# Kernel optimization log

Measured on AMD Instinct MI355X. Metric: run time of the kernel, lower is better.

Reference implementation:

```python
import jax, jax.numpy as jnp
import numpy as np

HIDDEN = 4096
N_HEADS = 16
HEAD_DIM = HIDDEN // N_HEADS  # 256
ROTARY_DIM = 64
ROPE_THETA = 10000.0


def _rope_cos_sin(positions):
    # positions: [S] int -> cos/sin: [S, ROTARY_DIM//2]
    inv_freq = 1.0 / (ROPE_THETA ** (jnp.arange(0, ROTARY_DIM, 2, dtype=jnp.float32) / ROTARY_DIM))
    angles = positions.astype(jnp.float32)[:, None] * inv_freq[None, :]
    return jnp.cos(angles), jnp.sin(angles)


def _apply_rope_interleaved(x, cos, sin):
    # x: [B, S, H, D]; rotate first ROTARY_DIM dims, GPT-J (non-neox) interleaved pairs
    xr = x[..., :ROTARY_DIM]
    x1 = xr[..., 0::2]
    x2 = xr[..., 1::2]
    c = cos[None, :, None, :]
    s = sin[None, :, None, :]
    o1 = x1 * c - x2 * s
    o2 = x1 * s + x2 * c
    rot = jnp.stack([o1, o2], axis=-1).reshape(xr.shape)
    return jnp.concatenate([rot, x[..., ROTARY_DIM:]], axis=-1)


def setup_inputs() -> dict:
    key = jax.random.key(0)
    k1, k2, k3 = jax.random.split(key, 3)
    B, S = 2, 2048
    hidden_states = jax.random.normal(k1, (B, S, HIDDEN), dtype=jnp.float32)
    positions = jnp.arange(S, dtype=jnp.int32)
    w_qkv = jax.random.normal(k2, (3 * HIDDEN, HIDDEN), dtype=jnp.float32) * 0.02
    w_out = jax.random.normal(k3, (HIDDEN, HIDDEN), dtype=jnp.float32) * 0.02
    return {"hidden_states": hidden_states, "positions": positions, "w_qkv": w_qkv, "w_out": w_out}


def reference(hidden_states, positions, w_qkv, w_out):
    B, S, H = hidden_states.shape
    qkv = jnp.einsum("bsh,oh->bso", hidden_states, w_qkv)  # [B,S,3H]
    q, k, v = jnp.split(qkv, 3, axis=-1)
    q = q.reshape(B, S, N_HEADS, HEAD_DIM)
    k = k.reshape(B, S, N_HEADS, HEAD_DIM)
    v = v.reshape(B, S, N_HEADS, HEAD_DIM)
    cos, sin = _rope_cos_sin(positions)
    q = _apply_rope_interleaved(q, cos, sin)
    k = _apply_rope_interleaved(k, cos, sin)
    scale = HEAD_DIM ** -0.5
    scores = jnp.einsum("bqhd,bkhd->bhqk", q, k) * scale  # [B,nh,S,S]
    causal = jnp.tril(jnp.ones((S, S), dtype=bool))
    scores = jnp.where(causal[None, None], scores, jnp.finfo(scores.dtype).min)
    probs = jax.nn.softmax(scores, axis=-1)
    attn = jnp.einsum("bhqk,bkhd->bqhd", probs, v).reshape(B, S, H)
    return jnp.einsum("bsh,oh->bso", attn, w_out)
```

## Files before the change

kernel.cpp:

```cpp
#include <hip/hip_runtime.h>

typedef __attribute__((ext_vector_type(8))) short short8;
typedef __attribute__((ext_vector_type(4))) float f32x4;

__device__ __forceinline__ unsigned short f2bf(float f) {
    union { float f; unsigned int u; } v; v.f = f;
    unsigned int u = v.u;
    unsigned int r = (u + 0x7FFFu + ((u >> 16) & 1u)) >> 16;
    return (unsigned short)r;
}
__device__ __forceinline__ float bf2f(unsigned short u) {
    union { unsigned int u; float f; } v; v.u = ((unsigned int)u) << 16;
    return v.f;
}
__device__ __forceinline__ void load_lds16(const void* g, void* l) {
    __builtin_amdgcn_global_load_lds(
        (const __attribute__((address_space(1))) void*)g,
        (__attribute__((address_space(3))) void*)l, 16, 0, 0);
}
#define BAR() asm volatile("s_barrier" ::: "memory")
#define WAITV(n) asm volatile("s_waitcnt vmcnt(" #n ")" ::: "memory")

__device__ __forceinline__ int swz(int o) { return o ^ ((o >> 3) & 0x70); }

__global__ __launch_bounds__(256) void conv_bf16(const float* __restrict__ in,
                                                 unsigned short* __restrict__ out, int n4) {
    int i = blockIdx.x * 256 + threadIdx.x;
    if (i >= n4) return;
    float4 v = ((const float4*)in)[i];
    ushort4 o;
    o.x = f2bf(v.x); o.y = f2bf(v.y); o.z = f2bf(v.z); o.w = f2bf(v.w);
    ((ushort4*)out)[i] = o;
}

template <bool OUT_BF16>
__global__ __launch_bounds__(512, 2) void gemm256(const unsigned short* __restrict__ A,
                                                  const unsigned short* __restrict__ B,
                                                  void* __restrict__ Cv,
                                                  int M, int N, int K, int NBN) {
    __shared__ __align__(16) char smem[131072];
    const int tid = threadIdx.x;
    const int lane = tid & 63, wv = tid >> 6;
    const int wm = wv >> 2, wn = wv & 3;
    const int fr = lane & 15, fo = (lane >> 4) * 8;

    const int nwg = gridDim.x, bid = blockIdx.x;
    const int q = nwg >> 3, r = nwg & 7, xcd = bid & 7, lid = bid >> 3;
    const int wg = (xcd < r ? xcd * (q + 1) : r * (q + 1) + (xcd - r) * q) + lid;
    const int bm = wg / NBN, bn = wg % NBN;

    const unsigned short* gA = A + (size_t)bm * 256 * K;
    const unsigned short* gB = B + (size_t)bn * 256 * K;

    int srow[2][2], scol[2][2];
#pragma unroll
    for (int h = 0; h < 2; ++h)
#pragma unroll
        for (int rr = 0; rr < 2; ++rr) {
            int o = h * 16384 + rr * 8192 + tid * 16;
            int osw = swz(o);
            srow[h][rr] = osw >> 7;
            scol[h][rr] = (osw & 127) >> 1;
        }

    f32x4 acc[8][4] = {};
    short8 a[4][2], b[4][2];

    auto STAGE = [&](const unsigned short* g, int regionBase, int h, int t) {
#pragma unroll
        for (int rr = 0; rr < 2; ++rr)
            load_lds16(g + (size_t)srow[h][rr] * K + t * 64 + scol[h][rr],
                       smem + regionBase + h * 16384 + rr * 8192 + tid * 16);
    };
    auto RDA = [&](int bufBase, int mh) {
#pragma unroll
        for (int mf = 0; mf < 4; ++mf)
#pragma unroll
            for (int ks = 0; ks < 2; ++ks) {
                int o = swz((wm * 128 + mh * 64 + mf * 16 + fr) * 128 + (ks * 32 + fo) * 2);
                a[mf][ks] = *(const short8*)(smem + bufBase + o);
            }
    };
    auto RDB = [&](int bufBase, int nh) {
#pragma unroll
        for (int jj = 0; jj < 2; ++jj)
#pragma unroll
            for (int ks = 0; ks < 2; ++ks) {
                int o = swz((wn * 64 + (nh * 2 + jj) * 16 + fr) * 128 + (ks * 32 + fo) * 2);
                b[nh * 2 + jj][ks] = *(const short8*)(smem + bufBase + 32768 + o);
            }
    };
    auto MM = [&](int mh, int nh) {
        __builtin_amdgcn_s_setprio(1);
#pragma unroll
        for (int mf = 0; mf < 4; ++mf)
#pragma unroll
            for (int jj = 0; jj < 2; ++jj)
#pragma unroll
                for (int ks = 0; ks < 2; ++ks)
                    acc[mh * 4 + mf][nh * 2 + jj] = __builtin_amdgcn_mfma_f32_16x16x32_bf16(
                        a[mf][ks], b[nh * 2 + jj][ks], acc[mh * 4 + mf][nh * 2 + jj], 0, 0, 0);
        __builtin_amdgcn_s_setprio(0);
    };

    const int A0 = 0, B0 = 32768, A1 = 65536, B1 = 98304;

    STAGE(gA, A0, 0, 0); STAGE(gA, A0, 1, 0);
    STAGE(gB, B0, 0, 0); STAGE(gB, B0, 1, 0);
    STAGE(gB, B1, 0, 1); STAGE(gB, B1, 1, 1);
    STAGE(gA, A1, 0, 1); STAGE(gA, A1, 1, 1);
    WAITV(8);
    BAR();
    RDA(A0, 0);
    RDB(A0, 0);

    const int NIT = K >> 7;
    for (int i = 0; i < NIT; ++i) {
        const bool last = (i == NIT - 1);
        const int t2 = 2 * i + 2, t3 = 2 * i + 3;
        RDB(A0, 1);
        MM(0, 0);
        if (i > 0) STAGE(gA, A1, 1, 2 * i + 1);
        BAR();
        MM(0, 1);
        RDA(A0, 1);
        BAR();
        MM(1, 1);
        if (!last) {
            STAGE(gB, B0, 0, t2);
            WAITV(2);
        } else {
            WAITV(0);
        }
        BAR();
        MM(1, 0);
        RDA(A1, 0); RDB(A1, 0);
        if (!last) { STAGE(gB, B0, 1, t2); STAGE(gA, A0, 0, t2); }
        BAR();
        RDB(A1, 1);
        MM(0, 0);
        if (!last) STAGE(gA, A0, 1, t2);
        BAR();
        MM(0, 1);
        RDA(A1, 1);
        BAR();
        MM(1, 1);
        if (!last) {
            STAGE(gB, B1, 0, t3);
            WAITV(2);
        }
        BAR();
        MM(1, 0);
        if (!last) {
            RDA(A0, 0); RDB(A0, 0);
            STAGE(gB, B1, 1, t3); STAGE(gA, A1, 0, t3);
        }
        BAR();
    }

    const size_t row0 = (size_t)bm * 256 + wm * 128 + ((lane >> 4) << 2);
    const int col0 = bn * 256 + wn * 64 + fr;
#pragma unroll
    for (int mf = 0; mf < 8; ++mf)
#pragma unroll
        for (int nf = 0; nf < 4; ++nf)
#pragma unroll
            for (int j = 0; j < 4; ++j) {
                size_t idx = (row0 + mf * 16 + j) * (size_t)N + col0 + nf * 16;
                if (OUT_BF16) ((unsigned short*)Cv)[idx] = f2bf(acc[mf][nf][j]);
                else          ((float*)Cv)[idx] = acc[mf][nf][j];
            }
}

__global__ __launch_bounds__(256) void rope_repack(const unsigned short* __restrict__ qkv,
                                                   const int* __restrict__ positions,
                                                   unsigned short* __restrict__ qp,
                                                   unsigned short* __restrict__ kp) {
    int r = blockIdx.x * 4 + (threadIdx.x >> 6);
    int h = r & 15, s = (r >> 4) & 2047, b = r >> 15;
    int d = (threadIdx.x & 63) * 4;
    const unsigned short* src = qkv + (size_t)(b * 2048 + s) * 12288 + h * 256 + d;
    ushort4 q = *(const ushort4*)src;
    ushort4 k = *(const ushort4*)(src + 4096);
    if (d < 64) {
        float pos = (float)positions[s];
        const float LF = 0.4152410118609203f;
        float i0 = (float)(d >> 1);
        float a0 = pos * exp2f(-i0 * LF);
        float a1 = pos * exp2f(-(i0 + 1.0f) * LF);
        float c0 = cosf(a0), s0 = sinf(a0), c1 = cosf(a1), s1 = sinf(a1);
        float qx = bf2f(q.x), qy = bf2f(q.y), qz = bf2f(q.z), qw = bf2f(q.w);
        q.x = f2bf(qx * c0 - qy * s0); q.y = f2bf(qx * s0 + qy * c0);
        q.z = f2bf(qz * c1 - qw * s1); q.w = f2bf(qz * s1 + qw * c1);
        float kx = bf2f(k.x), ky = bf2f(k.y), kz = bf2f(k.z), kw = bf2f(k.w);
        k.x = f2bf(kx * c0 - ky * s0); k.y = f2bf(kx * s0 + ky * c0);
        k.z = f2bf(kz * c1 - kw * s1); k.w = f2bf(kz * s1 + kw * c1);
    }
    size_t dst = ((size_t)((b * 16 + h) * 2048 + s)) * 256 + d;
    *(ushort4*)&qp[dst] = q;
    *(ushort4*)&kp[dst] = k;
}

__global__ __launch_bounds__(256) void v_transpose(const unsigned short* __restrict__ qkv,
                                                   unsigned short* __restrict__ vt) {
    int bid = blockIdx.x;
    int dt = bid & 3, st = (bid >> 2) & 31, bh = bid >> 7;
    int b = bh >> 4, h = bh & 15;
    __shared__ unsigned short t[64][72];
    int tid = threadIdx.x;
#pragma unroll
    for (int rep = 0; rep < 16; ++rep) {
        int idx = rep * 256 + tid;
        int r = idx >> 6, c = idx & 63;
        t[r][c] = qkv[(size_t)(b * 2048 + st * 64 + r) * 12288 + 8192 + h * 256 + dt * 64 + c];
    }
    __syncthreads();
#pragma unroll
    for (int rep = 0; rep < 16; ++rep) {
        int idx = rep * 256 + tid;
        int r = idx >> 6, c = idx & 63;
        vt[(size_t)(bh * 256 + dt * 64 + r) * 2048 + st * 64 + c] = t[c][r];
    }
}

__global__ __launch_bounds__(256) void attn_fwd(const unsigned short* __restrict__ Qp,
                                                const unsigned short* __restrict__ Kp,
                                                const unsigned short* __restrict__ Vt,
                                                unsigned short* __restrict__ Oa) {
    __shared__ __align__(16) unsigned short Ks[32 * 256];
    __shared__ __align__(16) unsigned short Vs[256 * 32];
    __shared__ __align__(16) unsigned short Ps[4][16 * 32];
    const int tid = threadIdx.x, lane = tid & 63, wv = tid >> 6;
    const int bh = blockIdx.x, qt = blockIdx.y;
    const int fr = lane & 15, fo = (lane >> 4) * 8;
    const unsigned short* Qb = Qp + (size_t)bh * 2048 * 256;
    const unsigned short* Kb = Kp + (size_t)bh * 2048 * 256;
    const unsigned short* Vb = Vt + (size_t)bh * 256 * 2048;
    const int qbase = qt * 64 + wv * 16;

    short8 qf[8];
#pragma unroll
    for (int c = 0; c < 8; ++c)
        qf[c] = *(const short8*)&Qb[(size_t)(qbase + fr) * 256 + c * 32 + fo];

    f32x4 o_acc[16] = {};
    float m_run[4] = {-1e30f, -1e30f, -1e30f, -1e30f};
    float l_run[4] = {0.f, 0.f, 0.f, 0.f};

    const int nkv = qt * 64 + 64;
    for (int kv0 = 0; kv0 < nkv; kv0 += 32) {
#pragma unroll
        for (int i = 0; i < 4; ++i) {
            int eb = (wv * 4 + i) * 512;
            load_lds16(&Kb[(size_t)(kv0 + (eb >> 8) + (lane >> 5)) * 256 + (lane & 31) * 8], &Ks[eb]);
        }
#pragma unroll
        for (int i = 0; i < 4; ++i) {
            int eb = (wv * 4 + i) * 512;
            load_lds16(&Vb[(size_t)((eb >> 5) + (lane >> 2)) * 2048 + kv0 + (lane & 3) * 8], &Vs[eb]);
        }
        __syncthreads();

        f32x4 sc[2] = {};
#pragma unroll
        for (int t = 0; t < 2; ++t)
#pragma unroll
            for (int c = 0; c < 8; ++c) {
                short8 kf = *(const short8*)&Ks[(t * 16 + fr) * 256 + c * 32 + fo];
                sc[t] = __builtin_amdgcn_mfma_f32_16x16x32_bf16(qf[c], kf, sc[t], 0, 0, 0);
            }

        float sv[2][4];
#pragma unroll
        for (int j = 0; j < 4; ++j) {
            int qi = qbase + ((lane >> 4) << 2) + j;
#pragma unroll
            for (int t = 0; t < 2; ++t) {
                float x = sc[t][j] * 0.0625f;
                int kvi = kv0 + t * 16 + fr;
                sv[t][j] = (kvi > qi) ? -1e30f : x;
            }
            float pm = fmaxf(sv[0][j], sv[1][j]);
#pragma unroll
            for (int off = 1; off < 16; off <<= 1)
                pm = fmaxf(pm, __shfl_xor(pm, off));
            float mn = fmaxf(m_run[j], pm);
            float al = __expf(m_run[j] - mn);
            m_run[j] = mn;
            float rs = 0.f;
#pragma unroll
            for (int t = 0; t < 2; ++t) {
                float p = __expf(sv[t][j] - mn);
                rs += p;
                Ps[wv][(((lane >> 4) << 2) + j) * 32 + t * 16 + fr] = f2bf(p);
            }
#pragma unroll
            for (int off = 1; off < 16; off <<= 1)
                rs += __shfl_xor(rs, off);
            l_run[j] = l_run[j] * al + rs;
#pragma unroll
            for (int n = 0; n < 16; ++n) o_acc[n][j] *= al;
        }

        short8 pf = *(const short8*)&Ps[wv][fr * 32 + fo];
#pragma unroll
        for (int n = 0; n < 16; ++n) {
            short8 vf = *(const short8*)&Vs[(n * 16 + fr) * 32 + fo];
            o_acc[n] = __builtin_amdgcn_mfma_f32_16x16x32_bf16(pf, vf, o_acc[n], 0, 0, 0);
        }
        __syncthreads();
    }

    const int b = bh >> 4, h = bh & 15;
#pragma unroll
    for (int j = 0; j < 4; ++j) {
        float inv = 1.0f / l_run[j];
        int qrow = qbase + ((lane >> 4) << 2) + j;
        size_t base = ((size_t)(b * 2048 + qrow)) * 4096 + h * 256;
#pragma unroll
        for (int n = 0; n < 16; ++n)
            Oa[base + n * 16 + fr] = f2bf(o_acc[n][j] * inv);
    }
}

extern "C" void kernel_launch(void* const* d_in, const int* in_sizes, int n_in,
                              void* d_out, int out_size, void* d_ws, size_t ws_size,
                              hipStream_t stream) {
    const float* hidden = (const float*)d_in[0];
    const int* positions = (const int*)d_in[1];
    const float* w_qkv = (const float*)d_in[2];
    const float* w_out = (const float*)d_in[3];
    float* out = (float*)d_out;

    const size_t MB32 = 33554432;
    char* ws = (char*)d_ws;
    unsigned short* hidden_bf = (unsigned short*)ws;
    unsigned short* wqkv_bf   = (unsigned short*)(ws + MB32);
    unsigned short* qkv_bf    = (unsigned short*)(ws + 4 * MB32);
    unsigned short* qp  = wqkv_bf;
    unsigned short* kp  = wqkv_bf + 16777216;
    unsigned short* vtp = wqkv_bf + 33554432;
    unsigned short* attn_bf = hidden_bf;
    unsigned short* wout_bf = qkv_bf;

    conv_bf16<<<16384, 256, 0, stream>>>(hidden, hidden_bf, 4194304);
    conv_bf16<<<49152, 256, 0, stream>>>(w_qkv, wqkv_bf, 12582912);

    gemm256<true><<<16 * 48, 512, 0, stream>>>(hidden_bf, wqkv_bf, qkv_bf, 4096, 12288, 4096, 48);

    rope_repack<<<16384, 256, 0, stream>>>(qkv_bf, positions, qp, kp);
    v_transpose<<<4096, 256, 0, stream>>>(qkv_bf, vtp);

    attn_fwd<<<dim3(32, 32), 256, 0, stream>>>(qp, kp, vtp, attn_bf);

    conv_bf16<<<16384, 256, 0, stream>>>(w_out, wout_bf, 4194304);
    gemm256<false><<<16 * 16, 512, 0, stream>>>(attn_bf, wout_bf, out, 4096, 4096, 4096, 16);
}
```

Measured before the change: 867.2 us.

## Swizzle K/V LDS tiles and skip online-softmax rescale when max barely grows

After: 861.6 us. About the same (-0.6%).

```diff
diff --git a/kernel.cpp b/kernel.cpp
--- a/kernel.cpp
+++ b/kernel.cpp
@@ -251,13 +251,19 @@
     for (int kv0 = 0; kv0 < nkv; kv0 += 32) {
 #pragma unroll
         for (int i = 0; i < 4; ++i) {
-            int eb = (wv * 4 + i) * 512;
-            load_lds16(&Kb[(size_t)(kv0 + (eb >> 8) + (lane >> 5)) * 256 + (lane & 31) * 8], &Ks[eb]);
+            int ob = (wv * 4 + i) * 1024 + lane * 16;
+            int osw = ob ^ ((ob >> 5) & 0x70);
+            int row = kv0 + (ob >> 9);
+            load_lds16(&Kb[(size_t)row * 256 + ((osw & 511) >> 1)],
+                       (char*)Ks + (wv * 4 + i) * 1024);
         }
 #pragma unroll
         for (int i = 0; i < 4; ++i) {
-            int eb = (wv * 4 + i) * 512;
-            load_lds16(&Vb[(size_t)((eb >> 5) + (lane >> 2)) * 2048 + kv0 + (lane & 3) * 8], &Vs[eb]);
+            int ob = (wv * 4 + i) * 1024 + lane * 16;
+            int osw = ob ^ ((((ob >> 6) ^ (ob >> 8)) & 3) << 4);
+            int drow = ob >> 6;
+            load_lds16(&Vb[(size_t)drow * 2048 + kv0 + ((osw & 63) >> 1)],
+                       (char*)Vs + (wv * 4 + i) * 1024);
         }
         __syncthreads();
 
@@ -266,11 +272,13 @@
         for (int t = 0; t < 2; ++t)
 #pragma unroll
             for (int c = 0; c < 8; ++c) {
-                short8 kf = *(const short8*)&Ks[(t * 16 + fr) * 256 + c * 32 + fo];
+                int o = (t * 16 + fr) * 512 + (c * 32 + fo) * 2;
+                o ^= (o >> 5) & 0x70;
+                short8 kf = *(const short8*)((const char*)Ks + o);
                 sc[t] = __builtin_amdgcn_mfma_f32_16x16x32_bf16(qf[c], kf, sc[t], 0, 0, 0);
             }
 
-        float sv[2][4];
+        float sv[2][4], pm[4];
 #pragma unroll
         for (int j = 0; j < 4; ++j) {
             int qi = qbase + ((lane >> 4) << 2) + j;
@@ -280,32 +288,46 @@
                 int kvi = kv0 + t * 16 + fr;
                 sv[t][j] = (kvi > qi) ? -1e30f : x;
             }
-            float pm = fmaxf(sv[0][j], sv[1][j]);
+            float p = fmaxf(sv[0][j], sv[1][j]);
 #pragma unroll
             for (int off = 1; off < 16; off <<= 1)
-                pm = fmaxf(pm, __shfl_xor(pm, off));
-            float mn = fmaxf(m_run[j], pm);
-            float al = __expf(m_run[j] - mn);
-            m_run[j] = mn;
+                p = fmaxf(p, __shfl_xor(p, off));
+            pm[j] = p;
+        }
+        bool need = (pm[0] > m_run[0] + 8.f) | (pm[1] > m_run[1] + 8.f) |
+                    (pm[2] > m_run[2] + 8.f) | (pm[3] > m_run[3] + 8.f);
+        if (__any(need)) {
+#pragma unroll
+            for (int j = 0; j < 4; ++j) {
+                float mn = fmaxf(m_run[j], pm[j]);
+                float al = __expf(m_run[j] - mn);
+                m_run[j] = mn;
+                l_run[j] *= al;
+#pragma unroll
+                for (int n = 0; n < 16; ++n) o_acc[n][j] *= al;
+            }
+        }
+#pragma unroll
+        for (int j = 0; j < 4; ++j) {
             float rs = 0.f;
 #pragma unroll
             for (int t = 0; t < 2; ++t) {
-                float p = __expf(sv[t][j] - mn);
+                float p = __expf(sv[t][j] - m_run[j]);
                 rs += p;
                 Ps[wv][(((lane >> 4) << 2) + j) * 32 + t * 16 + fr] = f2bf(p);
             }
 #pragma unroll
             for (int off = 1; off < 16; off <<= 1)
                 rs += __shfl_xor(rs, off);
-            l_run[j] = l_run[j] * al + rs;
-#pragma unroll
-            for (int n = 0; n < 16; ++n) o_acc[n][j] *= al;
+            l_run[j] += rs;
         }
 
         short8 pf = *(const short8*)&Ps[wv][fr * 32 + fo];
 #pragma unroll
         for (int n = 0; n < 16; ++n) {
-            short8 vf = *(const short8*)&Vs[(n * 16 + fr) * 32 + fo];
+            int o = (n * 16 + fr) * 64 + fo * 2;
+            o ^= (((o >> 6) ^ (o >> 8)) & 3) << 4;
+            short8 vf = *(const short8*)((const char*)Vs + o);
             o_acc[n] = __builtin_amdgcn_mfma_f32_16x16x32_bf16(pf, vf, o_acc[n], 0, 0, 0);
         }
         __syncthreads();
```
